# Performance work log

Measured on AMD Instinct MI355X. Metric: run time of the kernel, lower is better.

Reference implementation:

```python
import jax, jax.numpy as jnp
import numpy as np

D = 1024      # model dim
H = 16        # heads
DH = 64       # dim per head (lucidrains default)
DEPTH = 6
MLP = 2048
P = 32
PD = 3 * P * P   # 3072
NC = 1000
B = 4         # packed sequences
N = 640       # tokens per packed sequence (incl. padding)
M = 18        # images per packed sequence
GRID = 8      # image_size // patch_size
SIZES = [(8,8),(8,8),(7,7),(7,7),(6,8),(8,6),(6,6),(5,7),(7,5),(5,5),(4,8),(8,4),(4,6),(6,4),(4,4),(3,5),(5,3),(3,3)]
SCALE = DH ** -0.5


def _pack_meta():
    hs, ws, ids = [], [], []
    for i, (h, w) in enumerate(SIZES):
        hh, ww = np.meshgrid(np.arange(h), np.arange(w), indexing='ij')
        hs.append(hh.ravel()); ws.append(ww.ravel()); ids.append(np.full(h * w, i))
    h = np.concatenate(hs); w = np.concatenate(ws); ii = np.concatenate(ids)
    pad = N - h.shape[0]
    h = np.pad(h, (0, pad)); w = np.pad(w, (0, pad))
    ii = np.pad(ii, (0, pad), constant_values=-1)  # padding tokens form their own block
    return (np.tile(h, (B, 1)).astype(np.int32),
            np.tile(w, (B, 1)).astype(np.int32),
            np.tile(ii, (B, 1)).astype(np.int32))


def _ln(x, g, b, eps=1e-5):
    m = x.mean(-1, keepdims=True)
    v = ((x - m) ** 2).mean(-1, keepdims=True)
    return (x - m) * jax.lax.rsqrt(v + eps) * g + b


def _heads(t):  # [b, n, H*DH] -> [b, H, n, DH]
    return t.reshape(t.shape[0], t.shape[1], H, DH).swapaxes(1, 2)


def _mha(q_in, kv_in, mask, Wq, Wkv, Wo, qn_g, qn_b, kn_g, kn_b):
    # NaViT attention: pre-norm applied by caller to q_in; per-head qk LayerNorm; no biases.
    q = _ln(_heads(q_in @ Wq), qn_g, qn_b)
    k, v = jnp.split(kv_in @ Wkv, 2, axis=-1)
    k = _ln(_heads(k), kn_g, kn_b)
    v = _heads(v)
    dots = jnp.einsum('bhid,bhjd->bhij', q, k) * SCALE
    dots = jnp.where(mask, dots, jnp.finfo(dots.dtype).min)
    o = jnp.einsum('bhij,bhjd->bhid', jax.nn.softmax(dots, axis=-1), v)
    o = o.swapaxes(1, 2).reshape(o.shape[0], -1, H * DH)
    return o @ Wo


def _forward(patches, pe_ln1_g, pe_ln1_b, W_pe, b_pe, pe_ln2_g, pe_ln2_b, pos_h, pos_w,
             ln1_g, ln1_b, qn_g, qn_b, kn_g, kn_b, Wq, Wkv, Wo, ln2_g, ln2_b,
             W1, b1, W2, b2, fin_g, fin_b, pool_q, pl_ln_g, pl_ln_b, pl_qn_g, pl_qn_b,
             pl_kn_g, pl_kn_b, pl_Wq, pl_Wkv, pl_Wo, head_g, head_b, W_head, b_head,
             h_idx, w_idx, image_ids):
    # patch embedding: LN -> Linear -> LN, then factorized 2D pos embed
    x = _ln(patches, pe_ln1_g, pe_ln1_b) @ W_pe + b_pe
    x = _ln(x, pe_ln2_g, pe_ln2_b)
    x = x + pos_h[h_idx] + pos_w[w_idx]
    # block-diagonal attention mask: tokens attend only within their own image
    blk = (image_ids[:, :, None] == image_ids[:, None, :])[:, None]  # [B,1,N,N]
    for l in range(DEPTH):
        xn = _ln(x, ln1_g[l], ln1_b[l])
        x = x + _mha(xn, xn, blk, Wq[l], Wkv[l], Wo[l], qn_g[l], qn_b[l], kn_g[l], kn_b[l])
        xn = _ln(x, ln2_g[l], ln2_b[l])
        x = x + jax.nn.gelu(xn @ W1[l] + b1[l], approximate=False) @ W2[l] + b2[l]
    x = _ln(x, fin_g, fin_b)
    # attention pooling: one learned query per packed image (context NOT re-normed, as in na_vit)
    queries = jnp.broadcast_to(pool_q, (B, M, D))
    qn = _ln(queries, pl_ln_g, pl_ln_b)
    pmask = (jnp.arange(M)[None, :, None] == image_ids[:, None, :])[:, None]  # [B,1,M,N]
    pooled = _mha(qn, x, pmask, pl_Wq, pl_Wkv, pl_Wo, pl_qn_g, pl_qn_b, pl_kn_g, pl_kn_b) + queries
    pooled = pooled.reshape(B * M, D)
    return _ln(pooled, head_g, head_b) @ W_head + b_head  # [B*M, 1000]


def setup_inputs() -> dict:
    key = jax.random.key(0)
    ks = iter(jax.random.split(key, 32))
    h_idx, w_idx, image_ids = _pack_meta()
    f32 = jnp.float32
    d = dict(
        patches=jax.random.normal(next(ks), (B, N, PD), f32),
        pe_ln1_g=jnp.ones((PD,), f32), pe_ln1_b=jnp.zeros((PD,), f32),
        W_pe=0.02 * jax.random.normal(next(ks), (PD, D), f32), b_pe=jnp.zeros((D,), f32),
        pe_ln2_g=jnp.ones((D,), f32), pe_ln2_b=jnp.zeros((D,), f32),
        pos_h=0.02 * jax.random.normal(next(ks), (GRID, D), f32),
        pos_w=0.02 * jax.random.normal(next(ks), (GRID, D), f32),
        ln1_g=jnp.ones((DEPTH, D), f32), ln1_b=jnp.zeros((DEPTH, D), f32),
        qn_g=jnp.ones((DEPTH, DH), f32), qn_b=jnp.zeros((DEPTH, DH), f32),
        kn_g=jnp.ones((DEPTH, DH), f32), kn_b=jnp.zeros((DEPTH, DH), f32),
        Wq=0.02 * jax.random.normal(next(ks), (DEPTH, D, H * DH), f32),
        Wkv=0.02 * jax.random.normal(next(ks), (DEPTH, D, 2 * H * DH), f32),
        Wo=0.02 * jax.random.normal(next(ks), (DEPTH, H * DH, D), f32),
        ln2_g=jnp.ones((DEPTH, D), f32), ln2_b=jnp.zeros((DEPTH, D), f32),
        W1=0.02 * jax.random.normal(next(ks), (DEPTH, D, MLP), f32), b1=jnp.zeros((DEPTH, MLP), f32),
        W2=0.02 * jax.random.normal(next(ks), (DEPTH, MLP, D), f32), b2=jnp.zeros((DEPTH, D), f32),
        fin_g=jnp.ones((D,), f32), fin_b=jnp.zeros((D,), f32),
        pool_q=0.02 * jax.random.normal(next(ks), (D,), f32),
        pl_ln_g=jnp.ones((D,), f32), pl_ln_b=jnp.zeros((D,), f32),
        pl_qn_g=jnp.ones((DH,), f32), pl_qn_b=jnp.zeros((DH,), f32),
        pl_kn_g=jnp.ones((DH,), f32), pl_kn_b=jnp.zeros((DH,), f32),
        pl_Wq=0.02 * jax.random.normal(next(ks), (D, H * DH), f32),
        pl_Wkv=0.02 * jax.random.normal(next(ks), (D, 2 * H * DH), f32),
        pl_Wo=0.02 * jax.random.normal(next(ks), (H * DH, D), f32),
        head_g=jnp.ones((D,), f32), head_b=jnp.zeros((D,), f32),
        W_head=0.02 * jax.random.normal(next(ks), (D, NC), f32), b_head=jnp.zeros((NC,), f32),
        h_idx=jnp.asarray(h_idx), w_idx=jnp.asarray(w_idx), image_ids=jnp.asarray(image_ids),
    )
    return d


def reference(patches, pe_ln1_g, pe_ln1_b, W_pe, b_pe, pe_ln2_g, pe_ln2_b, pos_h, pos_w,
              ln1_g, ln1_b, qn_g, qn_b, kn_g, kn_b, Wq, Wkv, Wo, ln2_g, ln2_b,
              W1, b1, W2, b2, fin_g, fin_b, pool_q, pl_ln_g, pl_ln_b, pl_qn_g, pl_qn_b,
              pl_kn_g, pl_kn_b, pl_Wq, pl_Wkv, pl_Wo, head_g, head_b, W_head, b_head,
              h_idx, w_idx, image_ids):
    return _forward(patches, pe_ln1_g, pe_ln1_b, W_pe, b_pe, pe_ln2_g, pe_ln2_b, pos_h, pos_w,
                    ln1_g, ln1_b, qn_g, qn_b, kn_g, kn_b, Wq, Wkv, Wo, ln2_g, ln2_b,
                    W1, b1, W2, b2, fin_g, fin_b, pool_q, pl_ln_g, pl_ln_b, pl_qn_g, pl_qn_b,
                    pl_kn_g, pl_kn_b, pl_Wq, pl_Wkv, pl_Wo, head_g, head_b, W_head, b_head,
                    h_idx, w_idx, image_ids)
```

## Files before the change

kernel.cpp:

```cpp
#include <hip/hip_runtime.h>
#include <cmath>

constexpr int kB = 4, kN = 640, kD = 1024, kH = 16, kDH = 64;
constexpr int kDepth = 6, kMLP = 2048, kPD = 3072, kNC = 1000, kM = 18;
constexpr float kScale = 0.125f;
constexpr float kNegInf = -3.4028235e38f;

typedef __bf16 bf16;
typedef __attribute__((ext_vector_type(8))) __bf16 bf16x8;
typedef __attribute__((ext_vector_type(4))) __bf16 bf16x4;
typedef __attribute__((ext_vector_type(4))) float f32x4;

#define AS1 __attribute__((address_space(1)))
#define AS3 __attribute__((address_space(3)))

__device__ __forceinline__ void gload16(const void* g, void* l) {
  __builtin_amdgcn_global_load_lds((AS1 void*)g, (AS3 void*)l, 16, 0, 0);
}

template <typename OT>
__global__ __launch_bounds__(256) void ln_kernel(
    const float* __restrict__ in, OT* __restrict__ out,
    const float* __restrict__ g, const float* __restrict__ b, int K) {
  const int row = blockIdx.x;
  const float* x = in + (size_t)row * K;
  OT* o = out + (size_t)row * K;
  float s = 0.f, s2 = 0.f;
  for (int d = threadIdx.x; d < K; d += 256) { float v = x[d]; s += v; s2 += v * v; }
#pragma unroll
  for (int off = 32; off; off >>= 1) { s += __shfl_down(s, off); s2 += __shfl_down(s2, off); }
  __shared__ float ls[4], ls2[4];
  __shared__ float sm, sr;
  const int wid = threadIdx.x >> 6, lane = threadIdx.x & 63;
  if (lane == 0) { ls[wid] = s; ls2[wid] = s2; }
  __syncthreads();
  if (threadIdx.x == 0) {
    float a = ls[0] + ls[1] + ls[2] + ls[3];
    float a2 = ls2[0] + ls2[1] + ls2[2] + ls2[3];
    float mean = a / K;
    float var = a2 / K - mean * mean;
    sm = mean; sr = rsqrtf(var + 1e-5f);
  }
  __syncthreads();
  const float mean = sm, r = sr;
  for (int d = threadIdx.x; d < K; d += 256)
    o[d] = (OT)((x[d] - mean) * r * g[d] + b[d]);
}

__global__ __launch_bounds__(256) void ln_pos_kernel(
    const float* __restrict__ in, float* __restrict__ out,
    const float* __restrict__ g, const float* __restrict__ b,
    const float* __restrict__ ph, const float* __restrict__ pw,
    const int* __restrict__ hi, const int* __restrict__ wi) {
  const int row = blockIdx.x;
  const float* x = in + (size_t)row * kD;
  float* o = out + (size_t)row * kD;
  float s = 0.f, s2 = 0.f;
  for (int d = threadIdx.x; d < kD; d += 256) { float v = x[d]; s += v; s2 += v * v; }
#pragma unroll
  for (int off = 32; off; off >>= 1) { s += __shfl_down(s, off); s2 += __shfl_down(s2, off); }
  __shared__ float ls[4], ls2[4];
  __shared__ float sm, sr;
  const int wid = threadIdx.x >> 6, lane = threadIdx.x & 63;
  if (lane == 0) { ls[wid] = s; ls2[wid] = s2; }
  __syncthreads();
  if (threadIdx.x == 0) {
    float a = ls[0] + ls[1] + ls[2] + ls[3];
    float a2 = ls2[0] + ls2[1] + ls2[2] + ls2[3];
    float mean = a / kD;
    float var = a2 / kD - mean * mean;
    sm = mean; sr = rsqrtf(var + 1e-5f);
  }
  __syncthreads();
  const float mean = sm, r = sr;
  const float* phr = ph + (size_t)hi[row] * kD;
  const float* pwr = pw + (size_t)wi[row] * kD;
  for (int d = threadIdx.x; d < kD; d += 256)
    o[d] = (x[d] - mean) * r * g[d] + b[d] + phr[d] + pwr[d];
}

__global__ __launch_bounds__(64) void headln_kernel(
    float* __restrict__ p, int stride,
    const float* __restrict__ g, const float* __restrict__ b) {
  const int blk = blockIdx.x;
  const int outer = blk / kH, h = blk % kH;
  float* x = p + (size_t)outer * stride + h * kDH;
  const int lane = threadIdx.x;
  float v = x[lane];
  float s = v, s2 = v * v;
#pragma unroll
  for (int off = 32; off; off >>= 1) { s += __shfl_xor(s, off); s2 += __shfl_xor(s2, off); }
  const float m = s * (1.f / kDH);
  const float var = s2 * (1.f / kDH) - m * m;
  const float r = rsqrtf(var + 1e-5f);
  x[lane] = (v - m) * r * g[lane] + b[lane];
}

__global__ __launch_bounds__(256) void wt_kernel(
    const float* __restrict__ W, bf16* __restrict__ WT, int K, int Ncol) {
  __shared__ float s[32][33];
  const int n0 = blockIdx.x * 32, k0 = blockIdx.y * 32;
  const int tx = threadIdx.x & 31, ty = threadIdx.x >> 5;
#pragma unroll
  for (int i = 0; i < 4; ++i) {
    const int k = ty + i * 8;
    s[k][tx] = (n0 + tx < Ncol) ? W[(size_t)(k0 + k) * Ncol + (n0 + tx)] : 0.f;
  }
  __syncthreads();
#pragma unroll
  for (int i = 0; i < 4; ++i) {
    const int n = ty + i * 8;
    WT[(size_t)(n0 + n) * K + (k0 + tx)] = (bf16)s[tx][n];
  }
}

template <int NI, bool OUT_BF, bool GELU>
__global__ __launch_bounds__(256) void gemm64_kernel(
    const bf16* __restrict__ A, const bf16* __restrict__ WT,
    float* __restrict__ Cf, bf16* __restrict__ Cb,
    const float* __restrict__ bias, const float* __restrict__ res,
    int K, int Ncol, int nbx) {
  constexpr int BN = NI * 32;
  __shared__ __align__(16) bf16 As[2][64 * 64];
  __shared__ __align__(16) bf16 Bs[2][BN * 64];
  const int tid = threadIdx.x, lane = tid & 63, wid = tid >> 6;
  const int wr = wid >> 1, wc = wid & 1;
  const int cpx = gridDim.x >> 3;
  const int swz = (blockIdx.x & 7) * cpx + (blockIdx.x >> 3);
  const int row0 = (swz / nbx) * 64, col0 = (swz % nbx) * BN;
  const int fr = lane & 15, fg = lane >> 4;
  f32x4 acc[2][NI] = {};
  bf16* sA = As[0]; bf16* sB = Bs[0];
  bf16* dA = As[1]; bf16* dB = Bs[1];

  auto stage = [&](bf16* tA, bf16* tB, int kt) {
#pragma unroll
    for (int i = 0; i < 2; ++i) {
      const int c = i * 256 + tid;
      const int r = c >> 3, ci = c & 7;
      gload16(A + (size_t)(row0 + r) * K + kt + ((ci ^ (r & 7)) * 8),
              tA + (i * 256 + wid * 64) * 8);
    }
#pragma unroll
    for (int i = 0; i < NI; ++i) {
      const int c = i * 256 + tid;
      const int r = c >> 3, ci = c & 7;
      gload16(WT + (size_t)(col0 + r) * K + kt + ((ci ^ (r & 7)) * 8),
              tB + (i * 256 + wid * 64) * 8);
    }
  };
  auto compute = [&](const bf16* tA, const bf16* tB) {
#pragma unroll
    for (int kk = 0; kk < 2; ++kk) {
      bf16x8 af[2], bfr[NI];
#pragma unroll
      for (int mi = 0; mi < 2; ++mi) {
        const int r = wr * 32 + mi * 16 + fr;
        af[mi] = *(const bf16x8*)(tA + r * 64 + (((kk * 4 + fg) ^ (r & 7)) * 8));
      }
#pragma unroll
      for (int ni = 0; ni < NI; ++ni) {
        const int r = wc * (NI * 16) + ni * 16 + fr;
        bfr[ni] = *(const bf16x8*)(tB + r * 64 + (((kk * 4 + fg) ^ (r & 7)) * 8));
      }
#pragma unroll
      for (int mi = 0; mi < 2; ++mi)
#pragma unroll
        for (int ni = 0; ni < NI; ++ni)
          acc[mi][ni] = __builtin_amdgcn_mfma_f32_16x16x32_bf16(af[mi], bfr[ni], acc[mi][ni], 0, 0, 0);
    }
  };

  const int NT = K >> 6;
  stage(sA, sB, 0);
  __syncthreads();
  for (int t = 1; t < NT; ++t) {
    stage(dA, dB, t * 64);
    compute(sA, sB);
    __syncthreads();
    bf16* u;
    u = sA; sA = dA; dA = u;
    u = sB; sB = dB; dB = u;
  }
  compute(sA, sB);

  const int rb = row0 + wr * 32 + fg * 4;
  const int cb = col0 + wc * (NI * 16) + fr;
#pragma unroll
  for (int mi = 0; mi < 2; ++mi) {
#pragma unroll
    for (int ni = 0; ni < NI; ++ni) {
      const int cc = cb + ni * 16;
      const float bb = bias ? bias[cc] : 0.f;
#pragma unroll
      for (int r = 0; r < 4; ++r) {
        const int rr = rb + mi * 16 + r;
        float v = acc[mi][ni][r] + bb;
        if (res) v += res[(size_t)rr * Ncol + cc];
        if (GELU) v = 0.5f * v * (1.f + erff(v * 0.70710678118654752f));
        if (OUT_BF) Cb[(size_t)rr * Ncol + cc] = (bf16)v;
        else        Cf[(size_t)rr * Ncol + cc] = v;
      }
    }
  }
}

template <bool OUT_BF>
__global__ __launch_bounds__(256) void gemm_tail_kernel(
    const bf16* __restrict__ A, const bf16* __restrict__ WT,
    float* __restrict__ Cf, bf16* __restrict__ Cb,
    const float* __restrict__ bias, const float* __restrict__ resv,
    int Mr, int K, int Nc, int ldc, int resmode) {
  __shared__ __align__(16) bf16 As[64][40];
  __shared__ __align__(16) bf16 Bs[128][40];
  const int tid = threadIdx.x;
  const int lane = tid & 63, wid = tid >> 6;
  const int row0 = blockIdx.y * 64, col0 = blockIdx.x * 128;
  f32x4 acc[4][2] = {};
  const int am = tid >> 2, ako = (tid & 3) * 8;
  const int fr = lane & 15, fg = (lane >> 4) * 8;
  for (int k0 = 0; k0 < K; k0 += 32) {
    if (row0 + am < Mr)
      *(bf16x8*)&As[am][ako] = *(const bf16x8*)(A + (size_t)(row0 + am) * K + k0 + ako);
    else {
      bf16x8 z = {};
      *(bf16x8*)&As[am][ako] = z;
    }
#pragma unroll
    for (int it = 0; it < 2; ++it) {
      const int c = it * 256 + tid;
      const int n = c >> 2, ko = (c & 3) * 8;
      *(bf16x8*)&Bs[n][ko] = *(const bf16x8*)(WT + (size_t)(col0 + n) * K + k0 + ko);
    }
    __syncthreads();
    bf16x8 af[4], bfr[2];
#pragma unroll
    for (int mi = 0; mi < 4; ++mi) af[mi] = *(const bf16x8*)&As[mi * 16 + fr][fg];
#pragma unroll
    for (int ni = 0; ni < 2; ++ni) bfr[ni] = *(const bf16x8*)&Bs[wid * 32 + ni * 16 + fr][fg];
#pragma unroll
    for (int mi = 0; mi < 4; ++mi)
#pragma unroll
      for (int ni = 0; ni < 2; ++ni)
        acc[mi][ni] = __builtin_amdgcn_mfma_f32_16x16x32_bf16(af[mi], bfr[ni], acc[mi][ni], 0, 0, 0);
    __syncthreads();
  }
  const int r4 = (lane >> 4) * 4;
  const int cc0 = col0 + wid * 32 + (lane & 15);
#pragma unroll
  for (int mi = 0; mi < 4; ++mi) {
#pragma unroll
    for (int ni = 0; ni < 2; ++ni) {
      const int cc = cc0 + ni * 16;
      if (cc >= Nc) continue;
#pragma unroll
      for (int r = 0; r < 4; ++r) {
        const int rr = row0 + mi * 16 + r4 + r;
        if (rr >= Mr) continue;
        float v = acc[mi][ni][r];
        if (bias) v += bias[cc];
        if (resmode == 1) v += resv[(size_t)rr * ldc + cc];
        else if (resmode == 2) v += resv[cc];
        if (OUT_BF) Cb[(size_t)rr * ldc + cc] = (bf16)v;
        else        Cf[(size_t)rr * ldc + cc] = v;
      }
    }
  }
}

__global__ __launch_bounds__(256) void attn_kernel(
    const float* __restrict__ qkv, const int* __restrict__ ids,
    const float* __restrict__ qg, const float* __restrict__ qb,
    const float* __restrict__ kg, const float* __restrict__ kb,
    bf16* __restrict__ o) {
  const int h = blockIdx.x, img = blockIdx.y, b = blockIdx.z;
  const int tid = threadIdx.x, lane = tid & 63, wid = tid >> 6;
  __shared__ __align__(16) bf16 Qs[64][72];
  __shared__ __align__(16) bf16 Ks[64][72];
  __shared__ __align__(16) bf16 Vt[64][72];
  __shared__ __align__(16) bf16 Ps[64][72];
  __shared__ int wlo[4], whi[4];
  __shared__ int sLo, sHi;
  {
    const int want = (img < kM) ? img : -1;
    int lo = kN, hi = -1;
    for (int j = tid; j < kN; j += 256) {
      if (ids[b * kN + j] == want) { lo = min(lo, j); hi = max(hi, j); }
    }
#pragma unroll
    for (int off = 32; off; off >>= 1) {
      lo = min(lo, __shfl_xor(lo, off));
      hi = max(hi, __shfl_xor(hi, off));
    }
    if (lane == 0) { wlo[wid] = lo; whi[wid] = hi; }
    __syncthreads();
    if (tid == 0) {
      sLo = min(min(wlo[0], wlo[1]), min(wlo[2], wlo[3]));
      sHi = max(max(whi[0], whi[1]), max(whi[2], whi[3]));
    }
    __syncthreads();
  }
  if (sHi < 0) return;
  const int start = sLo, T = sHi - sLo + 1;
  if (img == kM) {
    for (int j = start + wid; j <= sHi; j += 4)
      o[((size_t)(b * kN + j)) * kD + h * kDH + lane] = (bf16)0.f;
    return;
  }
  for (int ch = tid; ch < 1024; ch += 256) {
    const int r = ch >> 4, d0 = (ch & 15) * 4;
    if (r < T) {
      const float* base = qkv + ((size_t)(b * kN + start + r)) * 3072 + h * kDH + d0;
      const float4 qv = *(const float4*)(base);
      const float4 kv = *(const float4*)(base + 1024);
      const float4 vv = *(const float4*)(base + 2048);
      float sq = qv.x + qv.y + qv.z + qv.w;
      float sq2 = qv.x * qv.x + qv.y * qv.y + qv.z * qv.z + qv.w * qv.w;
      float sk = kv.x + kv.y + kv.z + kv.w;
      float sk2 = kv.x * kv.x + kv.y * kv.y + kv.z * kv.z + kv.w * kv.w;
#pragma unroll
      for (int off = 1; off < 16; off <<= 1) {
        sq += __shfl_xor(sq, off); sq2 += __shfl_xor(sq2, off);
        sk += __shfl_xor(sk, off); sk2 += __shfl_xor(sk2, off);
      }
      const float qm = sq * (1.f / 64);
      const float qr = rsqrtf(sq2 * (1.f / 64) - qm * qm + 1e-5f);
      const float km = sk * (1.f / 64);
      const float kr = rsqrtf(sk2 * (1.f / 64) - km * km + 1e-5f);
      const float qe[4] = {qv.x, qv.y, qv.z, qv.w};
      const float ke[4] = {kv.x, kv.y, kv.z, kv.w};
      bf16x4 qw, kw;
#pragma unroll
      for (int e = 0; e < 4; ++e) {
        qw[e] = (bf16)((qe[e] - qm) * qr * qg[d0 + e] + qb[d0 + e]);
        kw[e] = (bf16)((ke[e] - km) * kr * kg[d0 + e] + kb[d0 + e]);
      }
      *(bf16x4*)&Qs[r][d0] = qw;
      *(bf16x4*)&Ks[r][d0] = kw;
      Vt[d0 + 0][r] = (bf16)vv.x;
      Vt[d0 + 1][r] = (bf16)vv.y;
      Vt[d0 + 2][r] = (bf16)vv.z;
      Vt[d0 + 3][r] = (bf16)vv.w;
    } else {
      const bf16x4 z = {};
      *(bf16x4*)&Qs[r][d0] = z;
      *(bf16x4*)&Ks[r][d0] = z;
      Vt[d0 + 0][r] = (bf16)0.f;
      Vt[d0 + 1][r] = (bf16)0.f;
      Vt[d0 + 2][r] = (bf16)0.f;
      Vt[d0 + 3][r] = (bf16)0.f;
    }
  }
  __syncthreads();
  const int fr = lane & 15, fg = lane >> 4;
  const int r0 = wid * 16;
  f32x4 sacc[4] = {};
#pragma unroll
  for (int k0 = 0; k0 < 64; k0 += 32) {
    const bf16x8 aq = *(const bf16x8*)&Qs[r0 + fr][k0 + fg * 8];
#pragma unroll
    for (int ni = 0; ni < 4; ++ni) {
      const bf16x8 bk = *(const bf16x8*)&Ks[ni * 16 + fr][k0 + fg * 8];
      sacc[ni] = __builtin_amdgcn_mfma_f32_16x16x32_bf16(aq, bk, sacc[ni], 0, 0, 0);
    }
  }
  float inv[4];
#pragma unroll
  for (int r = 0; r < 4; ++r) {
    float mx = kNegInf;
#pragma unroll
    for (int ni = 0; ni < 4; ++ni) {
      const float s = (ni * 16 + fr < T) ? sacc[ni][r] * kScale : kNegInf;
      sacc[ni][r] = s;
      mx = fmaxf(mx, s);
    }
#pragma unroll
    for (int off = 1; off < 16; off <<= 1) mx = fmaxf(mx, __shfl_xor(mx, off));
    float sum = 0.f;
#pragma unroll
    for (int ni = 0; ni < 4; ++ni) {
      const float p = __expf(sacc[ni][r] - mx);
      sacc[ni][r] = p;
      sum += p;
    }
#pragma unroll
    for (int off = 1; off < 16; off <<= 1) sum += __shfl_xor(sum, off);
    inv[r] = 1.f / sum;
  }
#pragma unroll
  for (int ni = 0; ni < 4; ++ni)
#pragma unroll
    for (int r = 0; r < 4; ++r)
      Ps[r0 + fg * 4 + r][ni * 16 + fr] = (bf16)sacc[ni][r];
  f32x4 oacc[4] = {};
#pragma unroll
  for (int k0 = 0; k0 < 64; k0 += 32) {
    const bf16x8 ap = *(const bf16x8*)&Ps[r0 + fr][k0 + fg * 8];
#pragma unroll
    for (int ni = 0; ni < 4; ++ni) {
      const bf16x8 bv = *(const bf16x8*)&Vt[ni * 16 + fr][k0 + fg * 8];
      oacc[ni] = __builtin_amdgcn_mfma_f32_16x16x32_bf16(ap, bv, oacc[ni], 0, 0, 0);
    }
  }
#pragma unroll
  for (int r = 0; r < 4; ++r) {
    const int i = r0 + fg * 4 + r;
    if (i < T) {
      const size_t orow = ((size_t)(b * kN + start + i)) * kD + h * kDH;
      const float iv = inv[r];
#pragma unroll
      for (int ni = 0; ni < 4; ++ni)
        o[orow + ni * 16 + fr] = (bf16)(oacc[ni][r] * iv);
    }
  }
}

__global__ __launch_bounds__(64) void poolattn_kernel(
    const float* __restrict__ qp, const float* __restrict__ kv,
    const int* __restrict__ ids, bf16* __restrict__ o) {
  const int blk = blockIdx.x;
  const int h = blk % kH;
  const int bm = blk / kH;
  const int m = bm % kM, b = bm / kM;
  const int lane = threadIdx.x;
  __shared__ float sc[kN];
  __shared__ float qs[kDH];
  qs[lane] = qp[h * kDH + lane];
  __syncthreads();
  float mymax = kNegInf;
  int jmn = kN, jmx = -1;
  for (int j = lane; j < kN; j += 64) {
    const int idj = ids[b * kN + j];
    float s;
    if (idj == m) {
      const float* krow = kv + ((size_t)(b * kN + j)) * (2 * kD) + h * kDH;
      float dot = 0.f;
#pragma unroll
      for (int d = 0; d < kDH; ++d) dot += qs[d] * krow[d];
      s = dot * kScale;
      jmn = min(jmn, j); jmx = max(jmx, j);
    } else {
      s = kNegInf;
    }
    sc[j] = s;
    mymax = fmaxf(mymax, s);
  }
#pragma unroll
  for (int off = 32; off; off >>= 1) {
    mymax = fmaxf(mymax, __shfl_xor(mymax, off));
    jmn = min(jmn, __shfl_xor(jmn, off));
    jmx = max(jmx, __shfl_xor(jmx, off));
  }
  const int jlo = jmn, jhi = jmx + 1;
  float mysum = 0.f;
  for (int j = jlo + lane; j < jhi; j += 64) {
    const float p = __expf(sc[j] - mymax);
    sc[j] = p;
    mysum += p;
  }
#pragma unroll
  for (int off = 32; off; off >>= 1) mysum += __shfl_xor(mysum, off);
  const float inv = 1.f / mysum;
  __syncthreads();
  float acc = 0.f;
  const float* vptr = kv + ((size_t)(b * kN + jlo)) * (2 * kD) + kD + h * kDH + lane;
  for (int j = jlo; j < jhi; ++j, vptr += 2 * kD) acc += sc[j] * vptr[0];
  o[((size_t)(b * kM + m)) * kD + h * kDH + lane] = (bf16)(acc * inv);
}

extern "C" void kernel_launch(void* const* d_in, const int* in_sizes, int n_in,
                              void* d_out, int out_size, void* d_ws, size_t ws_size,
                              hipStream_t stream) {
  const float* patches  = (const float*)d_in[0];
  const float* pe_ln1_g = (const float*)d_in[1];
  const float* pe_ln1_b = (const float*)d_in[2];
  const float* W_pe     = (const float*)d_in[3];
  const float* b_pe     = (const float*)d_in[4];
  const float* pe_ln2_g = (const float*)d_in[5];
  const float* pe_ln2_b = (const float*)d_in[6];
  const float* pos_h    = (const float*)d_in[7];
  const float* pos_w    = (const float*)d_in[8];
  const float* ln1_g    = (const float*)d_in[9];
  const float* ln1_b    = (const float*)d_in[10];
  const float* qn_g     = (const float*)d_in[11];
  const float* qn_b     = (const float*)d_in[12];
  const float* kn_g     = (const float*)d_in[13];
  const float* kn_b     = (const float*)d_in[14];
  const float* Wq       = (const float*)d_in[15];
  const float* Wkv      = (const float*)d_in[16];
  const float* Wo       = (const float*)d_in[17];
  const float* ln2_g    = (const float*)d_in[18];
  const float* ln2_b    = (const float*)d_in[19];
  const float* W1       = (const float*)d_in[20];
  const float* b1       = (const float*)d_in[21];
  const float* W2       = (const float*)d_in[22];
  const float* b2       = (const float*)d_in[23];
  const float* fin_g    = (const float*)d_in[24];
  const float* fin_b    = (const float*)d_in[25];
  const float* pool_q   = (const float*)d_in[26];
  const float* pl_ln_g  = (const float*)d_in[27];
  const float* pl_ln_b  = (const float*)d_in[28];
  const float* pl_qn_g  = (const float*)d_in[29];
  const float* pl_qn_b  = (const float*)d_in[30];
  const float* pl_kn_g  = (const float*)d_in[31];
  const float* pl_kn_b  = (const float*)d_in[32];
  const float* pl_Wq    = (const float*)d_in[33];
  const float* pl_Wkv   = (const float*)d_in[34];
  const float* pl_Wo    = (const float*)d_in[35];
  const float* head_g   = (const float*)d_in[36];
  const float* head_b   = (const float*)d_in[37];
  const float* W_head   = (const float*)d_in[38];
  const float* b_head   = (const float*)d_in[39];
  const int* h_idx      = (const int*)d_in[40];
  const int* w_idx      = (const int*)d_in[41];
  const int* image_ids  = (const int*)d_in[42];
  float* out = (float*)d_out;

  const size_t SZ = (size_t)kB * kN * kD;
  char* p = (char*)d_ws;
  float* x    = (float*)p;           p += SZ * 4;
  bf16*  xnb  = (bf16*)p;            p += SZ * 2;
  char*  scratch = p;                p += (SZ * 14);
  bf16*  wtbuf = (bf16*)p;           p += (size_t)kPD * kD * 2;
  char*  smalls = p;
  float* qkvb  = (float*)scratch;
  bf16*  attno = (bf16*)(scratch + SZ * 12);
  bf16*  plnb  = (bf16*)scratch;
  float* emb   = (float*)(scratch + SZ * 8);
  bf16*  h1b   = (bf16*)scratch;
  float* kvpool = (float*)scratch;
  bf16*  qn_vecb = (bf16*)smalls;
  float* qpool   = (float*)(smalls + 4096);
  bf16*  opoolb  = (bf16*)(smalls + 4096 + 4096);
  float* pooled  = (float*)(smalls + 4096 + 4096 + 147456 + 8192);
  bf16*  pooledn = (bf16*)((char*)pooled + 72 * 1024 * 4 + 8192);

  const int BN = kB * kN;
  const int nbyM = BN / 64;

  auto wt = [&](const float* W, bf16* WT, int K, int Ncol, int Npad) {
    wt_kernel<<<dim3(Npad / 32, K / 32), 256, 0, stream>>>(W, WT, K, Ncol);
  };

  ln_kernel<bf16><<<BN, 256, 0, stream>>>(patches, plnb, pe_ln1_g, pe_ln1_b, kPD);
  wt(W_pe, wtbuf, kPD, kD, kD);
  gemm64_kernel<2, false, false><<<(kD / 64) * nbyM, 256, 0, stream>>>(
      plnb, wtbuf, emb, nullptr, b_pe, nullptr, kPD, kD, kD / 64);
  ln_pos_kernel<<<BN, 256, 0, stream>>>(emb, x, pe_ln2_g, pe_ln2_b, pos_h, pos_w, h_idx, w_idx);

  for (int l = 0; l < kDepth; ++l) {
    ln_kernel<bf16><<<BN, 256, 0, stream>>>(x, xnb, ln1_g + (size_t)l * kD, ln1_b + (size_t)l * kD, kD);
    wt(Wq + (size_t)l * kD * kD, wtbuf, kD, kD, kD);
    wt(Wkv + (size_t)l * kD * 2 * kD, wtbuf + (size_t)kD * kD, kD, 2 * kD, 2 * kD);
    gemm64_kernel<4, false, false><<<(3 * kD / 128) * nbyM, 256, 0, stream>>>(
        xnb, wtbuf, qkvb, nullptr, nullptr, nullptr, kD, 3 * kD, 3 * kD / 128);
    attn_kernel<<<dim3(kH, kM + 1, kB), 256, 0, stream>>>(
        qkvb, image_ids,
        qn_g + (size_t)l * kDH, qn_b + (size_t)l * kDH,
        kn_g + (size_t)l * kDH, kn_b + (size_t)l * kDH, attno);
    wt(Wo + (size_t)l * kD * kD, wtbuf, kD, kD, kD);
    gemm64_kernel<2, false, false><<<(kD / 64) * nbyM, 256, 0, stream>>>(
        attno, wtbuf, x, nullptr, nullptr, x, kD, kD, kD / 64);
    ln_kernel<bf16><<<BN, 256, 0, stream>>>(x, xnb, ln2_g + (size_t)l * kD, ln2_b + (size_t)l * kD, kD);
    wt(W1 + (size_t)l * kD * kMLP, wtbuf, kD, kMLP, kMLP);
    gemm64_kernel<4, true, true><<<(kMLP / 128) * nbyM, 256, 0, stream>>>(
        xnb, wtbuf, nullptr, h1b, b1 + (size_t)l * kMLP, nullptr, kD, kMLP, kMLP / 128);
    wt(W2 + (size_t)l * kMLP * kD, wtbuf, kMLP, kD, kD);
    gemm64_kernel<2, false, false><<<(kD / 64) * nbyM, 256, 0, stream>>>(
        h1b, wtbuf, x, nullptr, b2 + (size_t)l * kD, x, kMLP, kD, kD / 64);
  }

  ln_kernel<bf16><<<BN, 256, 0, stream>>>(x, xnb, fin_g, fin_b, kD);

  ln_kernel<bf16><<<1, 256, 0, stream>>>(pool_q, qn_vecb, pl_ln_g, pl_ln_b, kD);
  wt(pl_Wq, wtbuf, kD, kD, kD);
  gemm_tail_kernel<false><<<dim3(8, 1), 256, 0, stream>>>(
      qn_vecb, wtbuf, qpool, nullptr, nullptr, nullptr, 1, kD, kD, kD, 0);
  headln_kernel<<<kH, 64, 0, stream>>>(qpool, kD, pl_qn_g, pl_qn_b);
  wt(pl_Wkv, wtbuf, kD, 2 * kD, 2 * kD);
  gemm64_kernel<4, false, false><<<(2 * kD / 128) * nbyM, 256, 0, stream>>>(
      xnb, wtbuf, kvpool, nullptr, nullptr, nullptr, kD, 2 * kD, 2 * kD / 128);
  headln_kernel<<<BN * kH, 64, 0, stream>>>(kvpool, 2 * kD, pl_kn_g, pl_kn_b);
  poolattn_kernel<<<kB * kM * kH, 64, 0, stream>>>(qpool, kvpool, image_ids, opoolb);
  wt(pl_Wo, wtbuf, kD, kD, kD);
  gemm_tail_kernel<false><<<dim3(8, 2), 256, 0, stream>>>(
      opoolb, wtbuf, pooled, nullptr, nullptr, pool_q, kB * kM, kD, kD, kD, 2);

  ln_kernel<bf16><<<kB * kM, 256, 0, stream>>>(pooled, pooledn, head_g, head_b, kD);
  wt(W_head, wtbuf, kD, kNC, 1024);
  gemm_tail_kernel<false><<<dim3(8, 2), 256, 0, stream>>>(
      pooledn, wtbuf, out, nullptr, b_head, nullptr, kB * kM, kD, kNC, kNC, 0);
}
```

Baseline: 1.118 ms.

## Batch all weight transposes into one launch, bf16 QKV, fused pool-query kernel

Replaces roughly 35 separate weight transpose/convert launches with one batched kernel that writes every layer's bf16 transposed weights to a persistent buffer. The QKV projection now stores its output in bf16 instead of fp32, which halves that traffic, and the attention kernel loads it with 8-wide bf16 vectors. The LayerNorm kernels are vectorised with float4. The pooling-query LN, GEMM and head LN are fused into a single small kernel. The cost is a larger weight workspace and lower QKV precision before the qk-LayerNorm.

```diff
diff --git a/kernel.cpp b/kernel.cpp
--- a/kernel.cpp
+++ b/kernel.cpp
@@ -16,6 +16,66 @@
 
 __device__ __forceinline__ void gload16(const void* g, void* l) {
   __builtin_amdgcn_global_load_lds((AS1 void*)g, (AS3 void*)l, 16, 0, 0);
+}
+
+constexpr size_t kMEG = 1048576;
+constexpr size_t kOffPe = 0;
+constexpr size_t kLayer0 = 3 * kMEG;
+constexpr size_t kLayerSz = 8 * kMEG;
+constexpr size_t kOffPool = kLayer0 + 6 * kLayerSz;
+constexpr size_t kOffPlWq = kOffPool;
+constexpr size_t kOffPlWkv = kOffPool + 1 * kMEG;
+constexpr size_t kOffPlWo = kOffPool + 3 * kMEG;
+constexpr size_t kOffHead = kOffPool + 4 * kMEG;
+constexpr size_t kWtTotal = kOffHead + 1 * kMEG;
+
+__global__ __launch_bounds__(256) void wt_all_kernel(
+    const float* __restrict__ pe, const float* __restrict__ wq,
+    const float* __restrict__ wkv, const float* __restrict__ wo,
+    const float* __restrict__ w1, const float* __restrict__ w2,
+    const float* __restrict__ plq, const float* __restrict__ plkv,
+    const float* __restrict__ plo, const float* __restrict__ whead,
+    bf16* __restrict__ WTB) {
+  const int j = blockIdx.y;
+  const float* W;
+  size_t doff;
+  int K, Nc, Np;
+  if (j == 0) {
+    W = pe; K = 3072; Nc = 1024; Np = 1024; doff = kOffPe;
+  } else if (j < 31) {
+    const int l = (j - 1) / 5, w = (j - 1) % 5;
+    const size_t lbase = kLayer0 + (size_t)l * kLayerSz;
+    switch (w) {
+      case 0:  W = wq  + (size_t)l * kMEG;     K = 1024; Nc = 1024; doff = lbase;            break;
+      case 1:  W = wkv + (size_t)l * 2 * kMEG; K = 1024; Nc = 2048; doff = lbase + kMEG;     break;
+      case 2:  W = wo  + (size_t)l * kMEG;     K = 1024; Nc = 1024; doff = lbase + 3 * kMEG; break;
+      case 3:  W = w1  + (size_t)l * 2 * kMEG; K = 1024; Nc = 2048; doff = lbase + 4 * kMEG; break;
+      default: W = w2  + (size_t)l * 2 * kMEG; K = 2048; Nc = 1024; doff = lbase + 6 * kMEG; break;
+    }
+    Np = Nc;
+  } else if (j == 31) { W = plq;  K = 1024; Nc = 1024; Np = 1024; doff = kOffPlWq; }
+  else if (j == 32)   { W = plkv; K = 1024; Nc = 2048; Np = 2048; doff = kOffPlWkv; }
+  else if (j == 33)   { W = plo;  K = 1024; Nc = 1024; Np = 1024; doff = kOffPlWo; }
+  else                { W = whead; K = 1024; Nc = 1000; Np = 1024; doff = kOffHead; }
+  const int nbx = Np >> 5;
+  const int ntiles = nbx * (K >> 5);
+  const int tile = blockIdx.x;
+  if (tile >= ntiles) return;
+  const int n0 = (tile % nbx) * 32, k0 = (tile / nbx) * 32;
+  bf16* WT = WTB + doff;
+  __shared__ float s[32][33];
+  const int tx = threadIdx.x & 31, ty = threadIdx.x >> 5;
+#pragma unroll
+  for (int i = 0; i < 4; ++i) {
+    const int k = ty + i * 8;
+    s[k][tx] = (n0 + tx < Nc) ? W[(size_t)(k0 + k) * Nc + (n0 + tx)] : 0.f;
+  }
+  __syncthreads();
+#pragma unroll
+  for (int i = 0; i < 4; ++i) {
+    const int n = ty + i * 8;
+    WT[(size_t)(n0 + n) * K + (k0 + tx)] = (bf16)s[tx][n];
+  }
 }
 
 template <typename OT>
@@ -25,8 +85,13 @@
   const int row = blockIdx.x;
   const float* x = in + (size_t)row * K;
   OT* o = out + (size_t)row * K;
+  const int K4 = K >> 2;
   float s = 0.f, s2 = 0.f;
-  for (int d = threadIdx.x; d < K; d += 256) { float v = x[d]; s += v; s2 += v * v; }
+  for (int c = threadIdx.x; c < K4; c += 256) {
+    const float4 v = ((const float4*)x)[c];
+    s += v.x + v.y + v.z + v.w;
+    s2 += v.x * v.x + v.y * v.y + v.z * v.z + v.w * v.w;
+  }
 #pragma unroll
   for (int off = 32; off; off >>= 1) { s += __shfl_down(s, off); s2 += __shfl_down(s2, off); }
   __shared__ float ls[4], ls2[4];
@@ -43,8 +108,16 @@
   }
   __syncthreads();
   const float mean = sm, r = sr;
-  for (int d = threadIdx.x; d < K; d += 256)
-    o[d] = (OT)((x[d] - mean) * r * g[d] + b[d]);
+  for (int c = threadIdx.x; c < K4; c += 256) {
+    const float4 v = ((const float4*)x)[c];
+    const float4 gv = ((const float4*)g)[c];
+    const float4 bv = ((const float4*)b)[c];
+    const int d = c * 4;
+    o[d + 0] = (OT)((v.x - mean) * r * gv.x + bv.x);
+    o[d + 1] = (OT)((v.y - mean) * r * gv.y + bv.y);
+    o[d + 2] = (OT)((v.z - mean) * r * gv.z + bv.z);
+    o[d + 3] = (OT)((v.w - mean) * r * gv.w + bv.w);
+  }
 }
 
 __global__ __launch_bounds__(256) void ln_pos_kernel(
@@ -56,7 +129,11 @@
   const float* x = in + (size_t)row * kD;
   float* o = out + (size_t)row * kD;
   float s = 0.f, s2 = 0.f;
-  for (int d = threadIdx.x; d < kD; d += 256) { float v = x[d]; s += v; s2 += v * v; }
+  for (int c = threadIdx.x; c < 256; c += 256) {
+    const float4 v = ((const float4*)x)[c];
+    s += v.x + v.y + v.z + v.w;
+    s2 += v.x * v.x + v.y * v.y + v.z * v.z + v.w * v.w;
+  }
 #pragma unroll
   for (int off = 32; off; off >>= 1) { s += __shfl_down(s, off); s2 += __shfl_down(s2, off); }
   __shared__ float ls[4], ls2[4];
@@ -73,10 +150,19 @@
   }
   __syncthreads();
   const float mean = sm, r = sr;
-  const float* phr = ph + (size_t)hi[row] * kD;
-  const float* pwr = pw + (size_t)wi[row] * kD;
-  for (int d = threadIdx.x; d < kD; d += 256)
-    o[d] = (x[d] - mean) * r * g[d] + b[d] + phr[d] + pwr[d];
+  const float4* phr = (const float4*)(ph + (size_t)hi[row] * kD);
+  const float4* pwr = (const float4*)(pw + (size_t)wi[row] * kD);
+  const int c = threadIdx.x;
+  const float4 v = ((const float4*)x)[c];
+  const float4 gv = ((const float4*)g)[c];
+  const float4 bv = ((const float4*)b)[c];
+  const float4 hv = phr[c], wv = pwr[c];
+  float4 ov;
+  ov.x = (v.x - mean) * r * gv.x + bv.x + hv.x + wv.x;
+  ov.y = (v.y - mean) * r * gv.y + bv.y + hv.y + wv.y;
+  ov.z = (v.z - mean) * r * gv.z + bv.z + hv.z + wv.z;
+  ov.w = (v.w - mean) * r * gv.w + bv.w + hv.w + wv.w;
+  ((float4*)o)[c] = ov;
 }
 
 __global__ __launch_bounds__(64) void headln_kernel(
@@ -96,21 +182,60 @@
   x[lane] = (v - m) * r * g[lane] + b[lane];
 }
 
-__global__ __launch_bounds__(256) void wt_kernel(
-    const float* __restrict__ W, bf16* __restrict__ WT, int K, int Ncol) {
-  __shared__ float s[32][33];
-  const int n0 = blockIdx.x * 32, k0 = blockIdx.y * 32;
-  const int tx = threadIdx.x & 31, ty = threadIdx.x >> 5;
-#pragma unroll
-  for (int i = 0; i < 4; ++i) {
-    const int k = ty + i * 8;
-    s[k][tx] = (n0 + tx < Ncol) ? W[(size_t)(k0 + k) * Ncol + (n0 + tx)] : 0.f;
-  }
-  __syncthreads();
-#pragma unroll
-  for (int i = 0; i < 4; ++i) {
-    const int n = ty + i * 8;
-    WT[(size_t)(n0 + n) * K + (k0 + tx)] = (bf16)s[tx][n];
+__global__ __launch_bounds__(256) void poolq_kernel(
+    const float* __restrict__ pq, const float* __restrict__ lg,
+    const float* __restrict__ lb, const bf16* __restrict__ WqT,
+    const float* __restrict__ qg, const float* __restrict__ qb,
+    float* __restrict__ qpool) {
+  const int h = blockIdx.x, tid = threadIdx.x;
+  __shared__ float qs[1024];
+  __shared__ float red[256];
+  __shared__ float ls[4], ls2[4];
+  __shared__ float sm, sr;
+  const float4 v = ((const float4*)pq)[tid];
+  float s = v.x + v.y + v.z + v.w;
+  float s2 = v.x * v.x + v.y * v.y + v.z * v.z + v.w * v.w;
+#pragma unroll
+  for (int off = 32; off; off >>= 1) { s += __shfl_down(s, off); s2 += __shfl_down(s2, off); }
+  const int wid = tid >> 6, lane = tid & 63;
+  if (lane == 0) { ls[wid] = s; ls2[wid] = s2; }
+  __syncthreads();
+  if (tid == 0) {
+    float a = ls[0] + ls[1] + ls[2] + ls[3];
+    float a2 = ls2[0] + ls2[1] + ls2[2] + ls2[3];
+    float mean = a / kD;
+    sm = mean; sr = rsqrtf(a2 / kD - mean * mean + 1e-5f);
+  }
+  __syncthreads();
+  {
+    const float mean = sm, r = sr;
+    const float4 gv = ((const float4*)lg)[tid];
+    const float4 bv = ((const float4*)lb)[tid];
+    qs[tid * 4 + 0] = (v.x - mean) * r * gv.x + bv.x;
+    qs[tid * 4 + 1] = (v.y - mean) * r * gv.y + bv.y;
+    qs[tid * 4 + 2] = (v.z - mean) * r * gv.z + bv.z;
+    qs[tid * 4 + 3] = (v.w - mean) * r * gv.w + bv.w;
+  }
+  __syncthreads();
+  const int d = tid & 63, qq = tid >> 6;
+  const bf16* wrow = WqT + (size_t)(h * 64 + d) * 1024 + qq * 256;
+  const float* qp = qs + qq * 256;
+  float part = 0.f;
+  for (int k = 0; k < 256; k += 8) {
+    const bf16x8 w8 = *(const bf16x8*)(wrow + k);
+#pragma unroll
+    for (int e = 0; e < 8; ++e) part += qp[k + e] * (float)w8[e];
+  }
+  red[tid] = part;
+  __syncthreads();
+  if (tid < 64) {
+    const float dot = red[tid] + red[tid + 64] + red[tid + 128] + red[tid + 192];
+    float hs = dot, hs2 = dot * dot;
+#pragma unroll
+    for (int off = 32; off; off >>= 1) { hs += __shfl_xor(hs, off); hs2 += __shfl_xor(hs2, off); }
+    const float m = hs * (1.f / kDH);
+    const float r = rsqrtf(hs2 * (1.f / kDH) - m * m + 1e-5f);
+    qpool[h * 64 + tid] = (dot - m) * r * qg[tid] + qb[tid];
   }
 }
 
@@ -269,7 +394,7 @@
 }
 
 __global__ __launch_bounds__(256) void attn_kernel(
-    const float* __restrict__ qkv, const int* __restrict__ ids,
+    const bf16* __restrict__ qkv, const int* __restrict__ ids,
     const float* __restrict__ qg, const float* __restrict__ qb,
     const float* __restrict__ kg, const float* __restrict__ kb,
     bf16* __restrict__ o) {
@@ -307,19 +432,25 @@
       o[((size_t)(b * kN + j)) * kD + h * kDH + lane] = (bf16)0.f;
     return;
   }
-  for (int ch = tid; ch < 1024; ch += 256) {
-    const int r = ch >> 4, d0 = (ch & 15) * 4;
+#pragma unroll
+  for (int it = 0; it < 2; ++it) {
+    const int ch = it * 256 + tid;
+    const int r = ch >> 3, d0 = (ch & 7) * 8;
     if (r < T) {
-      const float* base = qkv + ((size_t)(b * kN + start + r)) * 3072 + h * kDH + d0;
-      const float4 qv = *(const float4*)(base);
-      const float4 kv = *(const float4*)(base + 1024);
-      const float4 vv = *(const float4*)(base + 2048);
-      float sq = qv.x + qv.y + qv.z + qv.w;
-      float sq2 = qv.x * qv.x + qv.y * qv.y + qv.z * qv.z + qv.w * qv.w;
-      float sk = kv.x + kv.y + kv.z + kv.w;
-      float sk2 = kv.x * kv.x + kv.y * kv.y + kv.z * kv.z + kv.w * kv.w;
-#pragma unroll
-      for (int off = 1; off < 16; off <<= 1) {
+      const bf16* base = qkv + ((size_t)(b * kN + start + r)) * 3072 + h * kDH + d0;
+      const bf16x8 qv = *(const bf16x8*)(base);
+      const bf16x8 kv = *(const bf16x8*)(base + 1024);
+      const bf16x8 vv = *(const bf16x8*)(base + 2048);
+      float qf[8], kf[8];
+      float sq = 0.f, sq2 = 0.f, sk = 0.f, sk2 = 0.f;
+#pragma unroll
+      for (int e = 0; e < 8; ++e) {
+        qf[e] = (float)qv[e]; kf[e] = (float)kv[e];
+        sq += qf[e]; sq2 += qf[e] * qf[e];
+        sk += kf[e]; sk2 += kf[e] * kf[e];
+      }
+#pragma unroll
+      for (int off = 1; off < 8; off <<= 1) {
         sq += __shfl_xor(sq, off); sq2 += __shfl_xor(sq2, off);
         sk += __shfl_xor(sk, off); sk2 += __shfl_xor(sk2, off);
       }
@@ -327,28 +458,22 @@
       const float qr = rsqrtf(sq2 * (1.f / 64) - qm * qm + 1e-5f);
       const float km = sk * (1.f / 64);
       const float kr = rsqrtf(sk2 * (1.f / 64) - km * km + 1e-5f);
-      const float qe[4] = {qv.x, qv.y, qv.z, qv.w};
-      const float ke[4] = {kv.x, kv.y, kv.z, kv.w};
-      bf16x4 qw, kw;
-#pragma unroll
-      for (int e = 0; e < 4; ++e) {
-        qw[e] = (bf16)((qe[e] - qm) * qr * qg[d0 + e] + qb[d0 + e]);
-        kw[e] = (bf16)((ke[e] - km) * kr * kg[d0 + e] + kb[d0 + e]);
+      bf16x8 qw, kw;
+#pragma unroll
+      for (int e = 0; e < 8; ++e) {
+        qw[e] = (bf16)((qf[e] - qm) * qr * qg[d0 + e] + qb[d0 + e]);
+        kw[e] = (bf16)((kf[e] - km) * kr * kg[d0 + e] + kb[d0 + e]);
       }
-      *(bf16x4*)&Qs[r][d0] = qw;
-      *(bf16x4*)&Ks[r][d0] = kw;
-      Vt[d0 + 0][r] = (bf16)vv.x;
-      Vt[d0 + 1][r] = (bf16)vv.y;
-      Vt[d0 + 2][r] = (bf16)vv.z;
-      Vt[d0 + 3][r] = (bf16)vv.w;
+      *(bf16x8*)&Qs[r][d0] = qw;
+      *(bf16x8*)&Ks[r][d0] = kw;
+#pragma unroll
+      for (int e = 0; e < 8; ++e) Vt[d0 + e][r] = vv[e];
     } else {
-      const bf16x4 z = {};
-      *(bf16x4*)&Qs[r][d0] = z;
-      *(bf16x4*)&Ks[r][d0] = z;
-      Vt[d0 + 0][r] = (bf16)0.f;
-      Vt[d0 + 1][r] = (bf16)0.f;
-      Vt[d0 + 2][r] = (bf16)0.f;
-      Vt[d0 + 3][r] = (bf16)0.f;
+      const bf16x8 z = {};
+      *(bf16x8*)&Qs[r][d0] = z;
+      *(bf16x8*)&Ks[r][d0] = z;
+#pragma unroll
+      for (int e = 0; e < 8; ++e) Vt[d0 + e][r] = (bf16)0.f;
     }
   }
   __syncthreads();
@@ -520,74 +645,61 @@
   char* p = (char*)d_ws;
   float* x    = (float*)p;           p += SZ * 4;
   bf16*  xnb  = (bf16*)p;            p += SZ * 2;
-  char*  scratch = p;                p += (SZ * 14);
-  bf16*  wtbuf = (bf16*)p;           p += (size_t)kPD * kD * 2;
-  char*  smalls = p;
-  float* qkvb  = (float*)scratch;
-  bf16*  attno = (bf16*)(scratch + SZ * 12);
+  char*  scratch = p;                p += 32u * 1024 * 1024;
+  char*  smalls = p;                 p += 1u * 1024 * 1024;
+  bf16*  wtbuf = (bf16*)p;
+  bf16*  qkvbb = (bf16*)scratch;
+  bf16*  attno = (bf16*)(scratch + 16u * 1024 * 1024);
   bf16*  plnb  = (bf16*)scratch;
-  float* emb   = (float*)(scratch + SZ * 8);
+  float* emb   = (float*)(scratch + 16u * 1024 * 1024);
   bf16*  h1b   = (bf16*)scratch;
   float* kvpool = (float*)scratch;
-  bf16*  qn_vecb = (bf16*)smalls;
-  float* qpool   = (float*)(smalls + 4096);
-  bf16*  opoolb  = (bf16*)(smalls + 4096 + 4096);
-  float* pooled  = (float*)(smalls + 4096 + 4096 + 147456 + 8192);
-  bf16*  pooledn = (bf16*)((char*)pooled + 72 * 1024 * 4 + 8192);
+  float* qpool   = (float*)smalls;
+  bf16*  opoolb  = (bf16*)(smalls + 8192);
+  float* pooled  = (float*)(smalls + 8192 + 163840);
+  bf16*  pooledn = (bf16*)(smalls + 8192 + 163840 + 327680);
 
   const int BN = kB * kN;
   const int nbyM = BN / 64;
 
-  auto wt = [&](const float* W, bf16* WT, int K, int Ncol, int Npad) {
-    wt_kernel<<<dim3(Npad / 32, K / 32), 256, 0, stream>>>(W, WT, K, Ncol);
-  };
+  wt_all_kernel<<<dim3(3072, 35), 256, 0, stream>>>(
+      W_pe, Wq, Wkv, Wo, W1, W2, pl_Wq, pl_Wkv, pl_Wo, W_head, wtbuf);
 
   ln_kernel<bf16><<<BN, 256, 0, stream>>>(patches, plnb, pe_ln1_g, pe_ln1_b, kPD);
-  wt(W_pe, wtbuf, kPD, kD, kD);
   gemm64_kernel<2, false, false><<<(kD / 64) * nbyM, 256, 0, stream>>>(
-      plnb, wtbuf, emb, nullptr, b_pe, nullptr, kPD, kD, kD / 64);
+      plnb, wtbuf + kOffPe, emb, nullptr, b_pe, nullptr, kPD, kD, kD / 64);
   ln_pos_kernel<<<BN, 256, 0, stream>>>(emb, x, pe_ln2_g, pe_ln2_b, pos_h, pos_w, h_idx, w_idx);
 
   for (int l = 0; l < kDepth; ++l) {
+    const bf16* lw = wtbuf + kLayer0 + (size_t)l * kLayerSz;
     ln_kernel<bf16><<<BN, 256, 0, stream>>>(x, xnb, ln1_g + (size_t)l * kD, ln1_b + (size_t)l * kD, kD);
-    wt(Wq + (size_t)l * kD * kD, wtbuf, kD, kD, kD);
-    wt(Wkv + (size_t)l * kD * 2 * kD, wtbuf + (size_t)kD * kD, kD, 2 * kD, 2 * kD);
-    gemm64_kernel<4, false, false><<<(3 * kD / 128) * nbyM, 256, 0, stream>>>(
-        xnb, wtbuf, qkvb, nullptr, nullptr, nullptr, kD, 3 * kD, 3 * kD / 128);
+    gemm64_kernel<4, true, false><<<(3 * kD / 128) * nbyM, 256, 0, stream>>>(
+        xnb, lw, nullptr, qkvbb, nullptr, nullptr, kD, 3 * kD, 3 * kD / 128);
     attn_kernel<<<dim3(kH, kM + 1, kB), 256, 0, stream>>>(
-        qkvb, image_ids,
+        qkvbb, image_ids,
         qn_g + (size_t)l * kDH, qn_b + (size_t)l * kDH,
         kn_g + (size_t)l * kDH, kn_b + (size_t)l * kDH, attno);
-    wt(Wo + (size_t)l * kD * kD, wtbuf, kD, kD, kD);
     gemm64_kernel<2, false, false><<<(kD / 64) * nbyM, 256, 0, stream>>>(
-        attno, wtbuf, x, nullptr, nullptr, x, kD, kD, kD / 64);
+        attno, lw + 3 * kMEG, x, nullptr, nullptr, x, kD, kD, kD / 64);
     ln_kernel<bf16><<<BN, 256, 0, stream>>>(x, xnb, ln2_g + (size_t)l * kD, ln2_b + (size_t)l * kD, kD);
-    wt(W1 + (size_t)l * kD * kMLP, wtbuf, kD, kMLP, kMLP);
     gemm64_kernel<4, true, true><<<(kMLP / 128) * nbyM, 256, 0, stream>>>(
-        xnb, wtbuf, nullptr, h1b, b1 + (size_t)l * kMLP, nullptr, kD, kMLP, kMLP / 128);
-    wt(W2 + (size_t)l * kMLP * kD, wtbuf, kMLP, kD, kD);
+        xnb, lw + 4 * kMEG, nullptr, h1b, b1 + (size_t)l * kMLP, nullptr, kD, kMLP, kMLP / 128);
     gemm64_kernel<2, false, false><<<(kD / 64) * nbyM, 256, 0, stream>>>(
-        h1b, wtbuf, x, nullptr, b2 + (size_t)l * kD, x, kMLP, kD, kD / 64);
+        h1b, lw + 6 * kMEG, x, nullptr, b2 + (size_t)l * kD, x, kMLP, kD, kD / 64);
   }
 
   ln_kernel<bf16><<<BN, 256, 0, stream>>>(x, xnb, fin_g, fin_b, kD);
 
-  ln_kernel<bf16><<<1, 256, 0, stream>>>(pool_q, qn_vecb, pl_ln_g, pl_ln_b, kD);
-  wt(pl_Wq, wtbuf, kD, kD, kD);
-  gemm_tail_kernel<false><<<dim3(8, 1), 256, 0, stream>>>(
-      qn_vecb, wtbuf, qpool, nullptr, nullptr, nullptr, 1, kD, kD, kD, 0);
-  headln_kernel<<<kH, 64, 0, stream>>>(qpool, kD, pl_qn_g, pl_qn_b);
-  wt(pl_Wkv, wtbuf, kD, 2 * kD, 2 * kD);
+  poolq_kernel<<<kH, 256, 0, stream>>>(
+      pool_q, pl_ln_g, pl_ln_b, wtbuf + kOffPlWq, pl_qn_g, pl_qn_b, qpool);
   gemm64_kernel<4, false, false><<<(2 * kD / 128) * nbyM, 256, 0, stream>>>(
-      xnb, wtbuf, kvpool, nullptr, nullptr, nullptr, kD, 2 * kD, 2 * kD / 128);
+      xnb, wtbuf + kOffPlWkv, kvpool, nullptr, nullptr, nullptr, kD, 2 * kD, 2 * kD / 128);
   headln_kernel<<<BN * kH, 64, 0, stream>>>(kvpool, 2 * kD, pl_kn_g, pl_kn_b);
   poolattn_kernel<<<kB * kM * kH, 64, 0, stream>>>(qpool, kvpool, image_ids, opoolb);
-  wt(pl_Wo, wtbuf, kD, kD, kD);
   gemm_tail_kernel<false><<<dim3(8, 2), 256, 0, stream>>>(
-      opoolb, wtbuf, pooled, nullptr, nullptr, pool_q, kB * kM, kD, kD, kD, 2);
+      opoolb, wtbuf + kOffPlWo, pooled, nullptr, nullptr, pool_q, kB * kM, kD, kD, kD, 2);
 
   ln_kernel<bf16><<<kB * kM, 256, 0, stream>>>(pooled, pooledn, head_g, head_b, kD);
-  wt(W_head, wtbuf, kD, kNC, 1024);
   gemm_tail_kernel<false><<<dim3(8, 2), 256, 0, stream>>>(
-      pooledn, wtbuf, out, nullptr, b_head, nullptr, kB * kM, kD, kNC, kNC, 0);
-}
+      pooledn, wtbuf + kOffHead, out, nullptr, b_head, nullptr, kB * kM, kD, kNC, kNC, 0);
+}
```

New measurement: 1.018 ms. 8.9% less time.
